# Kernel tuning notes

Hardware: AMD Instinct MI355X
Metric: run time of the kernel (lower is better)

The kernel has to match this reference:

```python
import jax, jax.numpy as jnp
import numpy as np

NUM_LAYERS = 4
INFERENCE_STEPS = 8
LR_STATE = 0.1
B, S, D, V = 8, 512, 1024, 32000


def setup_inputs() -> dict:
    key = jax.random.key(0)
    ks = jax.random.split(key, 8)
    input_ids = jax.random.randint(ks[0], (B, S), 0, V)
    targets = jax.random.randint(ks[1], (B, S), 0, V)
    emb = jax.random.normal(ks[2], (V, D), dtype=jnp.float32) * 0.02
    # torch init: randn(output_dim, input_dim) * sqrt(2/output_dim)
    W_stack = jax.random.normal(ks[3], (NUM_LAYERS, D, D), dtype=jnp.float32) * np.float32(np.sqrt(2.0 / D))
    b_stack = jnp.zeros((NUM_LAYERS, D), dtype=jnp.float32)
    out_W = jax.random.normal(ks[4], (V, D), dtype=jnp.float32) * 0.02
    out_b = jnp.zeros((V,), dtype=jnp.float32)
    # initialize_states: randn latent state per PC layer
    states_init = jax.random.normal(ks[5], (NUM_LAYERS, B, S, D), dtype=jnp.float32)
    return {"input_ids": input_ids, "targets": targets, "emb": emb,
            "W_stack": W_stack, "b_stack": b_stack, "out_W": out_W,
            "out_b": out_b, "states_init": states_init}


def _predict(mu_higher, W, b):
    # F.linear(mu_higher, W, b) = mu_higher @ W^T + b, W: [out_dim(in layer terms input_dim), in_dim]
    return jnp.einsum('bsj,ij->bsi', mu_higher, W) + b


def reference(input_ids, targets, emb, W_stack, b_stack, out_W, out_b, states_init):
    L = NUM_LAYERS
    x = emb[input_ids]  # [B,S,D] input embeds = states[0] (fixed)

    def step(states, _):
        mu = [x] + [states[i] for i in range(L)]
        grads = []
        for l in range(1, L + 1):
            Wl, bl = W_stack[l - 1], b_stack[l - 1]
            eps_lower = mu[l - 1] - _predict(mu[l], Wl, bl)
            # grad_from_below = -F.linear(eps, W.t()) = -eps @ W
            g = -jnp.einsum('bsi,ij->bsj', eps_lower, Wl)
            if l < L:
                eps_self = mu[l] - _predict(mu[l + 1], W_stack[l], b_stack[l])
                g = g + eps_self
            grads.append(g)
        new_states = jnp.stack([states[i] - LR_STATE * grads[i] for i in range(L)])
        return new_states, None

    states, _ = jax.lax.scan(step, states_init, None, length=INFERENCE_STEPS)

    mu = [x] + [states[i] for i in range(L)]
    pc_losses = [jnp.mean((mu[l] - _predict(mu[l + 1], W_stack[l], b_stack[l])) ** 2) for l in range(L)]
    pc_loss = jnp.mean(jnp.stack(pc_losses))

    logits = jnp.einsum('bsd,vd->bsv', states[L - 1][:, :-1, :], out_W) + out_b  # [B,S-1,V]
    tgt = targets[:, 1:]
    logp = jax.nn.log_softmax(logits, axis=-1)
    ce = -jnp.mean(jnp.take_along_axis(logp, tgt[..., None], axis=-1))
    return jnp.stack([ce, pc_loss])
```

## Files before the change

### kernel.cpp

```cpp
#include <hip/hip_runtime.h>

typedef unsigned short u16;
typedef __attribute__((ext_vector_type(8))) __bf16 bf16x8;
typedef __attribute__((ext_vector_type(4))) float floatx4;

#define NUM_LAYERS 4
#define STEPS 8
#define LRS 0.1f
#define M_ROWS 4096
#define D_DIM 1024
#define V_DIM 32000
#define KDIM 1024
#define SM ((size_t)M_ROWS * D_DIM)
#define WM ((size_t)D_DIM * D_DIM)

__device__ __forceinline__ u16 f2b(float f) {
    union { float f; unsigned u; } c; c.f = f;
    unsigned u = c.u;
    u = (u + 0x7FFFu + ((u >> 16) & 1u)) >> 16;
    return (u16)u;
}
__device__ __forceinline__ float b2f(u16 b) {
    union { unsigned u; float f; } c; c.u = ((unsigned)b) << 16;
    return c.f;
}
__device__ __forceinline__ unsigned pk2(float a, float b) {
    return (unsigned)f2b(a) | ((unsigned)f2b(b) << 16);
}

__device__ __forceinline__ void ld16(const u16* g, u16* l) {
    __builtin_amdgcn_global_load_lds(
        (const __attribute__((address_space(1))) void*)g,
        (__attribute__((address_space(3))) void*)l, 16, 0, 0);
}

__device__ __forceinline__ void gemm_core(const u16* __restrict__ A,
                                          const u16* __restrict__ B,
                                          int m0, int n0,
                                          floatx4 (&acc)[4][4],
                                          u16* smem) {
    u16* a_lds = smem;
    u16* b_lds = smem + 8192;
    const int tid  = threadIdx.x;
    const int lane = tid & 63;
    const int wave = tid >> 6;
    const int wm = wave >> 1, wn = wave & 1;
    const int q = lane >> 4, lr = lane & 15;
    const int qs = q ^ ((lr >> 1) & 3);

    const int r0 = wave * 16 + (lane >> 2);
    const int cc = ((lane & 3) ^ ((lane >> 3) & 3)) * 8;
    const u16* ga = A + ((size_t)(m0 + r0) << 10) + cc;
    const u16* gb = B + ((size_t)(n0 + r0) << 10) + cc;
    u16* la = &a_lds[wave * 512];
    u16* lb = &b_lds[wave * 512];

    #pragma unroll
    for (int i = 0; i < 4; i++)
        #pragma unroll
        for (int j = 0; j < 4; j++)
            acc[i][j] = floatx4{0.f, 0.f, 0.f, 0.f};

    for (int kt = 0; kt < KDIM; kt += 64) {
        __syncthreads();
        ld16(ga + kt,                   la);
        ld16(ga + kt + 32,              la + 4096);
        ld16(ga + (64 << 10) + kt,      la + 2048);
        ld16(ga + (64 << 10) + kt + 32, la + 2048 + 4096);
        ld16(gb + kt,                   lb);
        ld16(gb + kt + 32,              lb + 4096);
        ld16(gb + (64 << 10) + kt,      lb + 2048);
        ld16(gb + (64 << 10) + kt + 32, lb + 2048 + 4096);
        __syncthreads();
        #pragma unroll
        for (int h = 0; h < 2; h++) {
            bf16x8 bfv[4];
            #pragma unroll
            for (int ni = 0; ni < 4; ni++)
                bfv[ni] = *(const bf16x8*)
                    &b_lds[h * 4096 + (wn * 64 + ni * 16 + lr) * 32 + qs * 8];
            #pragma unroll
            for (int mi = 0; mi < 4; mi++) {
                bf16x8 a = *(const bf16x8*)
                    &a_lds[h * 4096 + (wm * 64 + mi * 16 + lr) * 32 + qs * 8];
                #pragma unroll
                for (int ni = 0; ni < 4; ni++)
                    acc[mi][ni] = __builtin_amdgcn_mfma_f32_16x16x32_bf16(
                        a, bfv[ni], acc[mi][ni], 0, 0, 0);
            }
        }
    }
}


__global__ __launch_bounds__(256, 4) void eps_gemm_k(
        const u16* __restrict__ sbf, const u16* __restrict__ Wbf,
        const u16* __restrict__ xbf, const float* __restrict__ b_stack,
        u16* __restrict__ epsb, float* __restrict__ pc_accum) {
    __shared__ __align__(16) u16 smem[16384];
    const int z = blockIdx.z;
    const int m0 = blockIdx.y * 128, n0 = blockIdx.x * 128;
    floatx4 acc[4][4];
    gemm_core(sbf + (size_t)z * SM, Wbf + (size_t)z * WM, m0, n0, acc, smem);
    const u16* lower = (z == 0) ? xbf : (sbf + (size_t)(z - 1) * SM);
    const float* bias = b_stack + z * D_DIM;
    u16* eo = epsb + (size_t)z * SM;
    const int tid = threadIdx.x, lane = tid & 63, wave = tid >> 6;
    const int wm = wave >> 1, wn = wave & 1, q = lane >> 4, lr = lane & 15;
    float sq = 0.f;
    #pragma unroll
    for (int mi = 0; mi < 4; mi++) {
        __syncthreads();
        #pragma unroll
        for (int ni = 0; ni < 4; ni++) {
            const int col = wn * 64 + ni * 16 + lr;
            const float bc = bias[n0 + col];
            #pragma unroll
            for (int r = 0; r < 4; r++) {
                const int row = wm * 16 + q * 4 + r;
                const int scn = ((col >> 3) + ((row >> 2) & 3) * 4) & 15;
                smem[row * 128 + scn * 8 + (col & 7)] = f2b(acc[mi][ni][r] + bc);
            }
        }
        __syncthreads();
        #pragma unroll
        for (int h = 0; h < 2; h++) {
            const int c = tid + h * 256;
            const int lrow = c >> 4, ch = c & 15;
            const int scn = (ch + ((lrow >> 2) & 3) * 4) & 15;
            const int grow = m0 + (lrow >> 4) * 64 + mi * 16 + (lrow & 15);
            const size_t gidx = (size_t)grow * D_DIM + n0 + ch * 8;
            bf16x8 st = *(const bf16x8*)&smem[lrow * 128 + scn * 8];
            bf16x8 lo = *(const bf16x8*)(lower + gidx);
            float e[8];
            #pragma unroll
            for (int i = 0; i < 8; i++) e[i] = (float)lo[i] - (float)st[i];
            if (pc_accum) {
                #pragma unroll
                for (int i = 0; i < 8; i++) sq += e[i] * e[i];
            } else {
                uint4 ov;
                ov.x = pk2(e[0], e[1]); ov.y = pk2(e[2], e[3]);
                ov.z = pk2(e[4], e[5]); ov.w = pk2(e[6], e[7]);
                *(uint4*)(eo + gidx) = ov;
            }
        }
    }
    if (pc_accum) {
        #pragma unroll
        for (int off = 1; off < 64; off <<= 1) sq += __shfl_xor(sq, off, 64);
        __shared__ float ls[4];
        if (lane == 0) ls[wave] = sq;
        __syncthreads();
        if (tid == 0) atomicAdd(pc_accum, ls[0] + ls[1] + ls[2] + ls[3]);
    }
}

__global__ __launch_bounds__(256, 4) void upd_gemm_k(
        const u16* __restrict__ epsb, const u16* __restrict__ WTbf,
        u16* __restrict__ sbf) {
    __shared__ __align__(16) u16 smem[16384];
    const int z = blockIdx.z;
    const int m0 = blockIdx.y * 128, n0 = blockIdx.x * 128;
    floatx4 acc[4][4];
    gemm_core(epsb + (size_t)z * SM, WTbf + (size_t)z * WM, m0, n0, acc, smem);
    u16* Sb = sbf + (size_t)z * SM;
    const bool hn = (z < 3);
    const u16* en = epsb + (size_t)(hn ? (z + 1) : z) * SM;
    const int tid = threadIdx.x, lane = tid & 63, wave = tid >> 6;
    const int wm = wave >> 1, wn = wave & 1, q = lane >> 4, lr = lane & 15;
    #pragma unroll
    for (int mi = 0; mi < 4; mi++) {
        __syncthreads();
        #pragma unroll
        for (int ni = 0; ni < 4; ni++) {
            const int col = wn * 64 + ni * 16 + lr;
            #pragma unroll
            for (int r = 0; r < 4; r++) {
                const int row = wm * 16 + q * 4 + r;
                const int scn = ((col >> 3) + ((row >> 2) & 3) * 4) & 15;
                smem[row * 128 + scn * 8 + (col & 7)] = f2b(LRS * acc[mi][ni][r]);
            }
        }
        __syncthreads();
        #pragma unroll
        for (int h = 0; h < 2; h++) {
            const int c = tid + h * 256;
            const int lrow = c >> 4, ch = c & 15;
            const int scn = (ch + ((lrow >> 2) & 3) * 4) & 15;
            const int grow = m0 + (lrow >> 4) * 64 + mi * 16 + (lrow & 15);
            const size_t gidx = (size_t)grow * D_DIM + n0 + ch * 8;
            bf16x8 st = *(const bf16x8*)&smem[lrow * 128 + scn * 8];
            bf16x8 S8 = *(const bf16x8*)(Sb + gidx);
            float v[8];
            #pragma unroll
            for (int i = 0; i < 8; i++) v[i] = (float)S8[i] + (float)st[i];
            if (hn) {
                bf16x8 e8 = *(const bf16x8*)(en + gidx);
                #pragma unroll
                for (int i = 0; i < 8; i++) v[i] -= LRS * (float)e8[i];
            }
            uint4 ov;
            ov.x = pk2(v[0], v[1]); ov.y = pk2(v[2], v[3]);
            ov.z = pk2(v[4], v[5]); ov.w = pk2(v[6], v[7]);
            *(uint4*)(Sb + gidx) = ov;
        }
    }
}

__global__ __launch_bounds__(256, 4) void logits_k(
        const u16* __restrict__ s4bf, const u16* __restrict__ oWb,
        const float* __restrict__ out_b, const int* __restrict__ targets,
        float* __restrict__ part_m, float* __restrict__ part_s,
        float* __restrict__ tlog) {
    __shared__ __align__(16) u16 smem[16384];
    const int m0 = blockIdx.x * 128, n0 = blockIdx.y * 128;
    floatx4 acc[4][4];
    gemm_core(s4bf, oWb, m0, n0, acc, smem);
    __shared__ float redm[128][2];
    __shared__ float reds[128][2];
    const int tid = threadIdx.x, lane = tid & 63, wave = tid >> 6;
    const int wm = wave >> 1, wn = wave & 1, q = lane >> 4, lr = lane & 15;
    float ob[4];
    #pragma unroll
    for (int ni = 0; ni < 4; ni++) ob[ni] = out_b[n0 + wn * 64 + ni * 16 + lr];
    #pragma unroll
    for (int mi = 0; mi < 4; mi++) {
        #pragma unroll
        for (int r = 0; r < 4; r++) {
            const int grow = m0 + wm * 64 + mi * 16 + q * 4 + r;
            float l[4];
            #pragma unroll
            for (int ni = 0; ni < 4; ni++) l[ni] = acc[mi][ni][r] + ob[ni];
            if ((grow & 511) != 511) {
                const int t = targets[grow + 1];
                #pragma unroll
                for (int ni = 0; ni < 4; ni++) {
                    const int gcol = n0 + wn * 64 + ni * 16 + lr;
                    if (t == gcol) tlog[grow] = l[ni];
                }
            }
            float mx = fmaxf(fmaxf(l[0], l[1]), fmaxf(l[2], l[3]));
            #pragma unroll
            for (int off = 1; off < 16; off <<= 1)
                mx = fmaxf(mx, __shfl_xor(mx, off, 64));
            float sm = __expf(l[0] - mx) + __expf(l[1] - mx) +
                       __expf(l[2] - mx) + __expf(l[3] - mx);
            #pragma unroll
            for (int off = 1; off < 16; off <<= 1)
                sm += __shfl_xor(sm, off, 64);
            if (lr == 0) {
                const int rrow = wm * 64 + mi * 16 + q * 4 + r;
                redm[rrow][wn] = mx;
                reds[rrow][wn] = sm;
            }
        }
    }
    __syncthreads();
    if (tid < 128) {
        float ma = redm[tid][0], mb = redm[tid][1];
        float M = fmaxf(ma, mb);
        float S = reds[tid][0] * __expf(ma - M) + reds[tid][1] * __expf(mb - M);
        part_m[(size_t)blockIdx.y * M_ROWS + m0 + tid] = M;
        part_s[(size_t)blockIdx.y * M_ROWS + m0 + tid] = S;
    }
}

__global__ void gather_k(const int* __restrict__ ids,
                         const float* __restrict__ emb,
                         u16* __restrict__ xbf) {
    const int row = blockIdx.x;
    const int c = threadIdx.x * 4;
    float4 v = *(const float4*)(emb + (size_t)ids[row] * D_DIM + c);
    uint2 o; o.x = pk2(v.x, v.y); o.y = pk2(v.z, v.w);
    *(uint2*)(xbf + (size_t)row * D_DIM + c) = o;
}

__global__ void conv_w_k(const float* __restrict__ W,
                         u16* __restrict__ Wbf, u16* __restrict__ WTbf) {
    __shared__ float t[32][33];
    const int z = blockIdx.z;
    const int i = blockIdx.y * 32 + threadIdx.y;
    const int j = blockIdx.x * 32 + threadIdx.x;
    const float v = W[(size_t)z * WM + (size_t)i * D_DIM + j];
    Wbf[(size_t)z * WM + (size_t)i * D_DIM + j] = f2b(v);
    t[threadIdx.y][threadIdx.x] = v;
    __syncthreads();
    const int jo = blockIdx.x * 32 + threadIdx.y;
    const int io = blockIdx.y * 32 + threadIdx.x;
    WTbf[(size_t)z * WM + (size_t)jo * D_DIM + io] = f2b(t[threadIdx.x][threadIdx.y]);
}

__global__ void conv_outw_k(const float* __restrict__ oW, u16* __restrict__ oWb) {
    const size_t i = ((size_t)blockIdx.x * 256 + threadIdx.x) * 4;
    float4 v = *(const float4*)(oW + i);
    uint2 o; o.x = pk2(v.x, v.y); o.y = pk2(v.z, v.w);
    *(uint2*)(oWb + i) = o;
}

__global__ void init_states_k(const float* __restrict__ si,
                              u16* __restrict__ sbf) {
    const size_t i = ((size_t)blockIdx.x * 256 + threadIdx.x) * 4;
    float4 v = *(const float4*)(si + i);
    uint2 o; o.x = pk2(v.x, v.y); o.y = pk2(v.z, v.w);
    *(uint2*)(sbf + i) = o;
}

__global__ void ce_reduce_k(const float* __restrict__ part_m,
                            const float* __restrict__ part_s,
                            const float* __restrict__ tlog,
                            float* __restrict__ ce_sum) {
    const int row = blockIdx.x;
    if ((row & 511) == 511) return;
    const int tid = threadIdx.x;
    const int NT = V_DIM / 128;
    float m = -3.0e38f;
    for (int nt = tid; nt < NT; nt += 256)
        m = fmaxf(m, part_m[(size_t)nt * M_ROWS + row]);
    #pragma unroll
    for (int off = 1; off < 64; off <<= 1) m = fmaxf(m, __shfl_xor(m, off, 64));
    __shared__ float sm[4], ss[4];
    if ((tid & 63) == 0) sm[tid >> 6] = m;
    __syncthreads();
    m = fmaxf(fmaxf(sm[0], sm[1]), fmaxf(sm[2], sm[3]));
    float s = 0.f;
    for (int nt = tid; nt < NT; nt += 256)
        s += part_s[(size_t)nt * M_ROWS + row] *
             __expf(part_m[(size_t)nt * M_ROWS + row] - m);
    #pragma unroll
    for (int off = 1; off < 64; off <<= 1) s += __shfl_xor(s, off, 64);
    if ((tid & 63) == 0) ss[tid >> 6] = s;
    __syncthreads();
    if (tid == 0) {
        float loss = m + __logf(ss[0] + ss[1] + ss[2] + ss[3]) - tlog[row];
        atomicAdd(ce_sum, loss);
    }
}

__global__ void finalize_k(const float* __restrict__ scal, float* __restrict__ out) {
    out[0] = scal[0] / 4088.0f;
    out[1] = scal[1] / (float)(4 * SM);
}

extern "C" void kernel_launch(void* const* d_in, const int* in_sizes, int n_in,
                              void* d_out, int out_size, void* d_ws, size_t ws_size,
                              hipStream_t stream) {
    (void)in_sizes; (void)n_in; (void)out_size; (void)ws_size;
    const int*   ids = (const int*)d_in[0];
    const int*   tgt = (const int*)d_in[1];
    const float* emb = (const float*)d_in[2];
    const float* W   = (const float*)d_in[3];
    const float* bs  = (const float*)d_in[4];
    const float* oW  = (const float*)d_in[5];
    const float* ob  = (const float*)d_in[6];
    const float* si  = (const float*)d_in[7];

    char* ws = (char*)d_ws;
    u16*   sbf    = (u16*)  (ws + 0);
    u16*   epsb   = (u16*)  (ws + 33554432);
    u16*   xbf    = (u16*)  (ws + 67108864);
    u16*   Wbf    = (u16*)  (ws + 75497472);
    u16*   WTbf   = (u16*)  (ws + 83886080);
    u16*   oWb    = (u16*)  (ws + 92274688);
    float* part_m = (float*)(ws + 157810688);
    float* part_s = (float*)(ws + 161906688);
    float* tlog   = (float*)(ws + 166002688);
    float* scal   = (float*)(ws + 166019072);

    hipMemsetAsync(scal, 0, 256, stream);
    gather_k<<<M_ROWS, 256, 0, stream>>>(ids, emb, xbf);
    conv_w_k<<<dim3(32, 32, 4), dim3(32, 32), 0, stream>>>(W, Wbf, WTbf);
    conv_outw_k<<<(V_DIM * D_DIM) / 1024, 256, 0, stream>>>(oW, oWb);
    init_states_k<<<(4 * (int)SM) / 1024, 256, 0, stream>>>(si, sbf);

    for (int step = 0; step < STEPS; ++step) {
        eps_gemm_k<<<dim3(8, 32, 4), 256, 0, stream>>>(sbf, Wbf, xbf, bs, epsb,
                                                       nullptr);
        upd_gemm_k<<<dim3(8, 32, 4), 256, 0, stream>>>(epsb, WTbf, sbf);
    }
    eps_gemm_k<<<dim3(8, 32, 4), 256, 0, stream>>>(sbf, Wbf, xbf, bs, epsb,
                                                   scal + 1);
    logits_k<<<dim3(32, V_DIM / 128), 256, 0, stream>>>(sbf + 3 * SM, oWb, ob, tgt,
                                                        part_m, part_s, tlog);
    ce_reduce_k<<<M_ROWS, 256, 0, stream>>>(part_m, part_s, tlog, scal);
    finalize_k<<<1, 1, 0, stream>>>(scal, (float*)d_out);
}
```

Measured before the change: 1.573 ms.

## Switch GEMMs to 256x256 tiles with double-buffered LDS ping-pong pipeline

Replaces the 128x128 single-buffered GEMM core with a 256x256-tile, 512-thread core. It double-buffers LDS via direct global-to-LDS loads and interleaves A/B sub-tile staging with MFMA phases, using barriers, setprio and explicit waitcnts. The goal is more data reuse per loaded byte and load latency hidden behind compute. Epilogues now go through an fp32 LDS slab instead of bf16, which drops one rounding step. Logits partials are reduced over 256-wide column tiles. The risk is that eps/upd grids shrink to 256 blocks with low occupancy per CU, and LDS use per block grows to 128KB.

```diff
diff --git a/kernel.cpp b/kernel.cpp
--- a/kernel.cpp
+++ b/kernel.cpp
@@ -11,6 +11,8 @@
 #define D_DIM 1024
 #define V_DIM 32000
 #define KDIM 1024
+#define NK 16
+#define NTV (V_DIM / 256)
 #define SM ((size_t)M_ROWS * D_DIM)
 #define WM ((size_t)D_DIM * D_DIM)
 
@@ -34,210 +36,278 @@
         (__attribute__((address_space(3))) void*)l, 16, 0, 0);
 }
 
-__device__ __forceinline__ void gemm_core(const u16* __restrict__ A,
-                                          const u16* __restrict__ B,
-                                          int m0, int n0,
-                                          floatx4 (&acc)[4][4],
-                                          u16* smem) {
-    u16* a_lds = smem;
-    u16* b_lds = smem + 8192;
+__device__ __forceinline__ void gemm256(const u16* __restrict__ A,
+                                        const u16* __restrict__ B,
+                                        int m0, int n0,
+                                        floatx4 (&acc)[8][4],
+                                        u16* __restrict__ smem) {
     const int tid  = threadIdx.x;
-    const int lane = tid & 63;
-    const int wave = tid >> 6;
-    const int wm = wave >> 1, wn = wave & 1;
+    const int lane = tid & 63, wave = tid >> 6;
+    const int wm = wave >> 2, wn = wave & 3;
     const int q = lane >> 4, lr = lane & 15;
-    const int qs = q ^ ((lr >> 1) & 3);
-
-    const int r0 = wave * 16 + (lane >> 2);
-    const int cc = ((lane & 3) ^ ((lane >> 3) & 3)) * 8;
-    const u16* ga = A + ((size_t)(m0 + r0) << 10) + cc;
-    const u16* gb = B + ((size_t)(n0 + r0) << 10) + cc;
-    u16* la = &a_lds[wave * 512];
-    u16* lb = &b_lds[wave * 512];
-
-    #pragma unroll
-    for (int i = 0; i < 4; i++)
+
+    const int sr = tid >> 3;
+    const int sc = ((tid & 7) ^ (sr & 7)) * 8;
+    const u16* gA = A + (size_t)(m0 + sr) * KDIM + sc;
+    const u16* gB = B + (size_t)(n0 + sr) * KDIM + sc;
+    const int ldsw = wave * 512;
+
+    const int arow = wm * 128 + lr;
+    const int brow = wn * 64 + lr;
+    const int ck0 = ((q) ^ (lr & 7)) * 8;
+    const int ck1 = ((4 + q) ^ (lr & 7)) * 8;
+
+    #pragma unroll
+    for (int i = 0; i < 8; i++)
         #pragma unroll
         for (int j = 0; j < 4; j++)
             acc[i][j] = floatx4{0.f, 0.f, 0.f, 0.f};
 
-    for (int kt = 0; kt < KDIM; kt += 64) {
-        __syncthreads();
-        ld16(ga + kt,                   la);
-        ld16(ga + kt + 32,              la + 4096);
-        ld16(ga + (64 << 10) + kt,      la + 2048);
-        ld16(ga + (64 << 10) + kt + 32, la + 2048 + 4096);
-        ld16(gb + kt,                   lb);
-        ld16(gb + kt + 32,              lb + 4096);
-        ld16(gb + (64 << 10) + kt,      lb + 2048);
-        ld16(gb + (64 << 10) + kt + 32, lb + 2048 + 4096);
-        __syncthreads();
-        #pragma unroll
-        for (int h = 0; h < 2; h++) {
-            bf16x8 bfv[4];
-            #pragma unroll
-            for (int ni = 0; ni < 4; ni++)
-                bfv[ni] = *(const bf16x8*)
-                    &b_lds[h * 4096 + (wn * 64 + ni * 16 + lr) * 32 + qs * 8];
-            #pragma unroll
-            for (int mi = 0; mi < 4; mi++) {
-                bf16x8 a = *(const bf16x8*)
-                    &a_lds[h * 4096 + (wm * 64 + mi * 16 + lr) * 32 + qs * 8];
-                #pragma unroll
-                for (int ni = 0; ni < 4; ni++)
-                    acc[mi][ni] = __builtin_amdgcn_mfma_f32_16x16x32_bf16(
-                        a, bfv[ni], acc[mi][ni], 0, 0, 0);
-            }
-        }
-    }
-}
-
-
-__global__ __launch_bounds__(256, 4) void eps_gemm_k(
+#define STG(bufb, isB, ah, tt) do {                                          \
+        const u16* g_ = ((isB) ? gB : gA)                                    \
+            + (size_t)((ah) * 128) * KDIM + (size_t)(tt) * 64;               \
+        u16* d_ = smem + (bufb) * 32768 + (isB) * 16384 + (ah) * 8192 + ldsw;\
+        ld16(g_, d_);                                                        \
+        ld16(g_ + (size_t)64 * KDIM, d_ + 4096);                             \
+    } while (0)
+#define LDA_(mi, ck) (*(const bf16x8*)&smem[bufo + (arow + (mi) * 16) * 64 + (ck)])
+#define LDB_(ni, ck) (*(const bf16x8*)&smem[bufo + 16384 + (brow + (ni) * 16) * 64 + (ck)])
+
+    STG(0, 0, 0, 0); STG(0, 0, 1, 0);
+    STG(0, 1, 0, 0); STG(0, 1, 1, 0);
+    STG(1, 1, 0, 1); STG(1, 1, 1, 1);
+    asm volatile("s_waitcnt vmcnt(4)" ::: "memory");
+    __builtin_amdgcn_s_barrier();
+    __builtin_amdgcn_sched_barrier(0);
+
+    bf16x8 af[4][2], bf[4][2];
+
+    #pragma unroll 2
+    for (int t = 0; t < NK; ++t) {
+        const int bufo = (t & 1) * 32768;
+        const int nb = (t + 1) & 1;
+        #pragma unroll
+        for (int i = 0; i < 4; i++) { af[i][0] = LDA_(i, ck0); af[i][1] = LDA_(i, ck1); }
+        #pragma unroll
+        for (int j = 0; j < 2; j++) { bf[j][0] = LDB_(j, ck0); bf[j][1] = LDB_(j, ck1); }
+        if (t + 1 < NK) STG(nb, 0, 0, t + 1);
+        __builtin_amdgcn_s_barrier();
+        asm volatile("s_waitcnt lgkmcnt(0)" ::: "memory");
+        __builtin_amdgcn_sched_barrier(0);
+        __builtin_amdgcn_s_setprio(1);
+        #pragma unroll
+        for (int i = 0; i < 4; i++)
+            #pragma unroll
+            for (int j = 0; j < 2; j++) {
+                acc[i][j] = __builtin_amdgcn_mfma_f32_16x16x32_bf16(af[i][0], bf[j][0], acc[i][j], 0, 0, 0);
+                acc[i][j] = __builtin_amdgcn_mfma_f32_16x16x32_bf16(af[i][1], bf[j][1], acc[i][j], 0, 0, 0);
+            }
+        __builtin_amdgcn_s_setprio(0);
+        __builtin_amdgcn_sched_barrier(0);
+        __builtin_amdgcn_s_barrier();
+        __builtin_amdgcn_sched_barrier(0);
+        #pragma unroll
+        for (int j = 2; j < 4; j++) { bf[j][0] = LDB_(j, ck0); bf[j][1] = LDB_(j, ck1); }
+        if (t + 1 < NK) STG(nb, 0, 1, t + 1);
+        __builtin_amdgcn_s_barrier();
+        asm volatile("s_waitcnt lgkmcnt(0)" ::: "memory");
+        __builtin_amdgcn_sched_barrier(0);
+        __builtin_amdgcn_s_setprio(1);
+        #pragma unroll
+        for (int i = 0; i < 4; i++)
+            #pragma unroll
+            for (int j = 2; j < 4; j++) {
+                acc[i][j] = __builtin_amdgcn_mfma_f32_16x16x32_bf16(af[i][0], bf[j][0], acc[i][j], 0, 0, 0);
+                acc[i][j] = __builtin_amdgcn_mfma_f32_16x16x32_bf16(af[i][1], bf[j][1], acc[i][j], 0, 0, 0);
+            }
+        __builtin_amdgcn_s_setprio(0);
+        __builtin_amdgcn_sched_barrier(0);
+        __builtin_amdgcn_s_barrier();
+        __builtin_amdgcn_sched_barrier(0);
+        #pragma unroll
+        for (int i = 0; i < 4; i++) { af[i][0] = LDA_(4 + i, ck0); af[i][1] = LDA_(4 + i, ck1); }
+        if (t + 2 < NK) STG(t & 1, 1, 0, t + 2);
+        __builtin_amdgcn_s_barrier();
+        asm volatile("s_waitcnt lgkmcnt(0)" ::: "memory");
+        __builtin_amdgcn_sched_barrier(0);
+        __builtin_amdgcn_s_setprio(1);
+        #pragma unroll
+        for (int i = 0; i < 4; i++)
+            #pragma unroll
+            for (int j = 0; j < 2; j++) {
+                acc[4 + i][j] = __builtin_amdgcn_mfma_f32_16x16x32_bf16(af[i][0], bf[j][0], acc[4 + i][j], 0, 0, 0);
+                acc[4 + i][j] = __builtin_amdgcn_mfma_f32_16x16x32_bf16(af[i][1], bf[j][1], acc[4 + i][j], 0, 0, 0);
+            }
+        __builtin_amdgcn_s_setprio(0);
+        __builtin_amdgcn_sched_barrier(0);
+        __builtin_amdgcn_s_barrier();
+        __builtin_amdgcn_sched_barrier(0);
+        if (t + 2 < NK) STG(t & 1, 1, 1, t + 2);
+        __builtin_amdgcn_s_barrier();
+        __builtin_amdgcn_sched_barrier(0);
+        __builtin_amdgcn_s_setprio(1);
+        #pragma unroll
+        for (int i = 0; i < 4; i++)
+            #pragma unroll
+            for (int j = 2; j < 4; j++) {
+                acc[4 + i][j] = __builtin_amdgcn_mfma_f32_16x16x32_bf16(af[i][0], bf[j][0], acc[4 + i][j], 0, 0, 0);
+                acc[4 + i][j] = __builtin_amdgcn_mfma_f32_16x16x32_bf16(af[i][1], bf[j][1], acc[4 + i][j], 0, 0, 0);
+            }
+        __builtin_amdgcn_s_setprio(0);
+        __builtin_amdgcn_sched_barrier(0);
+        if (t + 2 < NK) { asm volatile("s_waitcnt vmcnt(4)" ::: "memory"); }
+        else            { asm volatile("s_waitcnt vmcnt(0)" ::: "memory"); }
+        __builtin_amdgcn_s_barrier();
+        __builtin_amdgcn_sched_barrier(0);
+    }
+#undef STG
+#undef LDA_
+#undef LDB_
+}
+
+#define SLAB_S 68
+
+__global__ __launch_bounds__(512, 2) void eps_gemm_k(
         const u16* __restrict__ sbf, const u16* __restrict__ Wbf,
         const u16* __restrict__ xbf, const float* __restrict__ b_stack,
         u16* __restrict__ epsb, float* __restrict__ pc_accum) {
-    __shared__ __align__(16) u16 smem[16384];
+    __shared__ __align__(16) u16 smem[65536];
     const int z = blockIdx.z;
-    const int m0 = blockIdx.y * 128, n0 = blockIdx.x * 128;
-    floatx4 acc[4][4];
-    gemm_core(sbf + (size_t)z * SM, Wbf + (size_t)z * WM, m0, n0, acc, smem);
+    const int m0 = blockIdx.y * 256, n0 = blockIdx.x * 256;
+    floatx4 acc[8][4];
+    gemm256(sbf + (size_t)z * SM, Wbf + (size_t)z * WM, m0, n0, acc, smem);
     const u16* lower = (z == 0) ? xbf : (sbf + (size_t)(z - 1) * SM);
     const float* bias = b_stack + z * D_DIM;
     u16* eo = epsb + (size_t)z * SM;
     const int tid = threadIdx.x, lane = tid & 63, wave = tid >> 6;
-    const int wm = wave >> 1, wn = wave & 1, q = lane >> 4, lr = lane & 15;
+    const int wm = wave >> 2, wn = wave & 3, q = lane >> 4, lr = lane & 15;
+    float* fp = (float*)smem;
+    const int row2 = tid >> 1, scb = (tid & 1) * 32;
     float sq = 0.f;
     #pragma unroll
-    for (int mi = 0; mi < 4; mi++) {
-        __syncthreads();
-        #pragma unroll
-        for (int ni = 0; ni < 4; ni++) {
-            const int col = wn * 64 + ni * 16 + lr;
-            const float bc = bias[n0 + col];
-            #pragma unroll
-            for (int r = 0; r < 4; r++) {
-                const int row = wm * 16 + q * 4 + r;
-                const int scn = ((col >> 3) + ((row >> 2) & 3) * 4) & 15;
-                smem[row * 128 + scn * 8 + (col & 7)] = f2b(acc[mi][ni][r] + bc);
+    for (int ni = 0; ni < 4; ++ni) {
+        __syncthreads();
+        #pragma unroll
+        for (int mi = 0; mi < 8; ++mi)
+            #pragma unroll
+            for (int r = 0; r < 4; ++r)
+                fp[(wm * 128 + mi * 16 + q * 4 + r) * SLAB_S + wn * 16 + lr] = acc[mi][ni][r];
+        __syncthreads();
+        const int grow = m0 + row2;
+        #pragma unroll
+        for (int j = 0; j < 8; ++j) {
+            const int sc_ = scb + j * 4;
+            float4 v = *(const float4*)&fp[row2 * SLAB_S + sc_];
+            const int gcol = n0 + (sc_ >> 4) * 64 + ni * 16 + (sc_ & 15);
+            const size_t gidx = (size_t)grow * D_DIM + gcol;
+            const float4 b4 = *(const float4*)&bias[gcol];
+            ushort4 lo4 = *(const ushort4*)(lower + gidx);
+            float e0 = b2f(lo4.x) - (v.x + b4.x);
+            float e1 = b2f(lo4.y) - (v.y + b4.y);
+            float e2 = b2f(lo4.z) - (v.z + b4.z);
+            float e3 = b2f(lo4.w) - (v.w + b4.w);
+            if (pc_accum) {
+                sq += e0 * e0 + e1 * e1 + e2 * e2 + e3 * e3;
+            } else {
+                uint2 ov; ov.x = pk2(e0, e1); ov.y = pk2(e2, e3);
+                *(uint2*)(eo + gidx) = ov;
             }
         }
-        __syncthreads();
-        #pragma unroll
-        for (int h = 0; h < 2; h++) {
-            const int c = tid + h * 256;
-            const int lrow = c >> 4, ch = c & 15;
-            const int scn = (ch + ((lrow >> 2) & 3) * 4) & 15;
-            const int grow = m0 + (lrow >> 4) * 64 + mi * 16 + (lrow & 15);
-            const size_t gidx = (size_t)grow * D_DIM + n0 + ch * 8;
-            bf16x8 st = *(const bf16x8*)&smem[lrow * 128 + scn * 8];
-            bf16x8 lo = *(const bf16x8*)(lower + gidx);
-            float e[8];
-            #pragma unroll
-            for (int i = 0; i < 8; i++) e[i] = (float)lo[i] - (float)st[i];
-            if (pc_accum) {
-                #pragma unroll
-                for (int i = 0; i < 8; i++) sq += e[i] * e[i];
-            } else {
-                uint4 ov;
-                ov.x = pk2(e[0], e[1]); ov.y = pk2(e[2], e[3]);
-                ov.z = pk2(e[4], e[5]); ov.w = pk2(e[6], e[7]);
-                *(uint4*)(eo + gidx) = ov;
-            }
+    }
+    if (pc_accum) {
+        #pragma unroll
+        for (int off = 1; off < 64; off <<= 1) sq += __shfl_xor(sq, off, 64);
+        __syncthreads();
+        if (lane == 0) fp[wave] = sq;
+        __syncthreads();
+        if (tid == 0) {
+            float s = 0.f;
+            #pragma unroll
+            for (int w = 0; w < 8; ++w) s += fp[w];
+            atomicAdd(pc_accum, s);
         }
     }
-    if (pc_accum) {
-        #pragma unroll
-        for (int off = 1; off < 64; off <<= 1) sq += __shfl_xor(sq, off, 64);
-        __shared__ float ls[4];
-        if (lane == 0) ls[wave] = sq;
-        __syncthreads();
-        if (tid == 0) atomicAdd(pc_accum, ls[0] + ls[1] + ls[2] + ls[3]);
-    }
-}
-
-__global__ __launch_bounds__(256, 4) void upd_gemm_k(
+}
+
+__global__ __launch_bounds__(512, 2) void upd_gemm_k(
         const u16* __restrict__ epsb, const u16* __restrict__ WTbf,
         u16* __restrict__ sbf) {
-    __shared__ __align__(16) u16 smem[16384];
+    __shared__ __align__(16) u16 smem[65536];
     const int z = blockIdx.z;
-    const int m0 = blockIdx.y * 128, n0 = blockIdx.x * 128;
-    floatx4 acc[4][4];
-    gemm_core(epsb + (size_t)z * SM, WTbf + (size_t)z * WM, m0, n0, acc, smem);
+    const int m0 = blockIdx.y * 256, n0 = blockIdx.x * 256;
+    floatx4 acc[8][4];
+    gemm256(epsb + (size_t)z * SM, WTbf + (size_t)z * WM, m0, n0, acc, smem);
     u16* Sb = sbf + (size_t)z * SM;
     const bool hn = (z < 3);
     const u16* en = epsb + (size_t)(hn ? (z + 1) : z) * SM;
     const int tid = threadIdx.x, lane = tid & 63, wave = tid >> 6;
-    const int wm = wave >> 1, wn = wave & 1, q = lane >> 4, lr = lane & 15;
-    #pragma unroll
-    for (int mi = 0; mi < 4; mi++) {
-        __syncthreads();
-        #pragma unroll
-        for (int ni = 0; ni < 4; ni++) {
-            const int col = wn * 64 + ni * 16 + lr;
-            #pragma unroll
-            for (int r = 0; r < 4; r++) {
-                const int row = wm * 16 + q * 4 + r;
-                const int scn = ((col >> 3) + ((row >> 2) & 3) * 4) & 15;
-                smem[row * 128 + scn * 8 + (col & 7)] = f2b(LRS * acc[mi][ni][r]);
-            }
+    const int wm = wave >> 2, wn = wave & 3, q = lane >> 4, lr = lane & 15;
+    float* fp = (float*)smem;
+    const int row2 = tid >> 1, scb = (tid & 1) * 32;
+    #pragma unroll
+    for (int ni = 0; ni < 4; ++ni) {
+        __syncthreads();
+        #pragma unroll
+        for (int mi = 0; mi < 8; ++mi)
+            #pragma unroll
+            for (int r = 0; r < 4; ++r)
+                fp[(wm * 128 + mi * 16 + q * 4 + r) * SLAB_S + wn * 16 + lr] = acc[mi][ni][r];
+        __syncthreads();
+        const int grow = m0 + row2;
+        #pragma unroll
+        for (int j = 0; j < 8; ++j) {
+            const int sc_ = scb + j * 4;
+            float4 v = *(const float4*)&fp[row2 * SLAB_S + sc_];
+            const int gcol = n0 + (sc_ >> 4) * 64 + ni * 16 + (sc_ & 15);
+            const size_t gidx = (size_t)grow * D_DIM + gcol;
+            ushort4 S8 = *(const ushort4*)(Sb + gidx);
+            float v0 = b2f(S8.x) + LRS * v.x;
+            float v1 = b2f(S8.y) + LRS * v.y;
+            float v2 = b2f(S8.z) + LRS * v.z;
+            float v3 = b2f(S8.w) + LRS * v.w;
+            if (hn) {
+                ushort4 e8 = *(const ushort4*)(en + gidx);
+                v0 -= LRS * b2f(e8.x); v1 -= LRS * b2f(e8.y);
+                v2 -= LRS * b2f(e8.z); v3 -= LRS * b2f(e8.w);
+            }
+            uint2 ov; ov.x = pk2(v0, v1); ov.y = pk2(v2, v3);
+            *(uint2*)(Sb + gidx) = ov;
         }
-        __syncthreads();
-        #pragma unroll
-        for (int h = 0; h < 2; h++) {
-            const int c = tid + h * 256;
-            const int lrow = c >> 4, ch = c & 15;
-            const int scn = (ch + ((lrow >> 2) & 3) * 4) & 15;
-            const int grow = m0 + (lrow >> 4) * 64 + mi * 16 + (lrow & 15);
-            const size_t gidx = (size_t)grow * D_DIM + n0 + ch * 8;
-            bf16x8 st = *(const bf16x8*)&smem[lrow * 128 + scn * 8];
-            bf16x8 S8 = *(const bf16x8*)(Sb + gidx);
-            float v[8];
-            #pragma unroll
-            for (int i = 0; i < 8; i++) v[i] = (float)S8[i] + (float)st[i];
-            if (hn) {
-                bf16x8 e8 = *(const bf16x8*)(en + gidx);
-                #pragma unroll
-                for (int i = 0; i < 8; i++) v[i] -= LRS * (float)e8[i];
-            }
-            uint4 ov;
-            ov.x = pk2(v[0], v[1]); ov.y = pk2(v[2], v[3]);
-            ov.z = pk2(v[4], v[5]); ov.w = pk2(v[6], v[7]);
-            *(uint4*)(Sb + gidx) = ov;
-        }
-    }
-}
-
-__global__ __launch_bounds__(256, 4) void logits_k(
+    }
+}
+
+__global__ __launch_bounds__(512, 2) void logits_k(
         const u16* __restrict__ s4bf, const u16* __restrict__ oWb,
         const float* __restrict__ out_b, const int* __restrict__ targets,
         float* __restrict__ part_m, float* __restrict__ part_s,
         float* __restrict__ tlog) {
-    __shared__ __align__(16) u16 smem[16384];
-    const int m0 = blockIdx.x * 128, n0 = blockIdx.y * 128;
-    floatx4 acc[4][4];
-    gemm_core(s4bf, oWb, m0, n0, acc, smem);
-    __shared__ float redm[128][2];
-    __shared__ float reds[128][2];
+    __shared__ __align__(16) u16 smem[65536];
+    const int m0 = blockIdx.x * 256, n0 = blockIdx.y * 256;
+    floatx4 acc[8][4];
+    gemm256(s4bf, oWb, m0, n0, acc, smem);
     const int tid = threadIdx.x, lane = tid & 63, wave = tid >> 6;
-    const int wm = wave >> 1, wn = wave & 1, q = lane >> 4, lr = lane & 15;
+    const int wm = wave >> 2, wn = wave & 3, q = lane >> 4, lr = lane & 15;
+    float* redm = (float*)smem;
+    float* reds = redm + 1024;
     float ob[4];
     #pragma unroll
-    for (int ni = 0; ni < 4; ni++) ob[ni] = out_b[n0 + wn * 64 + ni * 16 + lr];
-    #pragma unroll
-    for (int mi = 0; mi < 4; mi++) {
-        #pragma unroll
-        for (int r = 0; r < 4; r++) {
-            const int grow = m0 + wm * 64 + mi * 16 + q * 4 + r;
+    for (int ni = 0; ni < 4; ++ni) ob[ni] = out_b[n0 + wn * 64 + ni * 16 + lr];
+    __syncthreads();
+    #pragma unroll
+    for (int mi = 0; mi < 8; ++mi) {
+        #pragma unroll
+        for (int r = 0; r < 4; ++r) {
+            const int rrow = wm * 128 + mi * 16 + q * 4 + r;
+            const int grow = m0 + rrow;
             float l[4];
             #pragma unroll
             for (int ni = 0; ni < 4; ni++) l[ni] = acc[mi][ni][r] + ob[ni];
             if ((grow & 511) != 511) {
-                const int t = targets[grow + 1];
+                const int tg = targets[grow + 1];
                 #pragma unroll
                 for (int ni = 0; ni < 4; ni++) {
                     const int gcol = n0 + wn * 64 + ni * 16 + lr;
-                    if (t == gcol) tlog[grow] = l[ni];
+                    if (tg == gcol) tlog[grow] = l[ni];
                 }
             }
             float mx = fmaxf(fmaxf(l[0], l[1]), fmaxf(l[2], l[3]));
@@ -249,18 +319,16 @@
             #pragma unroll
             for (int off = 1; off < 16; off <<= 1)
                 sm += __shfl_xor(sm, off, 64);
-            if (lr == 0) {
-                const int rrow = wm * 64 + mi * 16 + q * 4 + r;
-                redm[rrow][wn] = mx;
-                reds[rrow][wn] = sm;
-            }
+            if (lr == 0) { redm[rrow * 4 + wn] = mx; reds[rrow * 4 + wn] = sm; }
         }
     }
     __syncthreads();
-    if (tid < 128) {
-        float ma = redm[tid][0], mb = redm[tid][1];
-        float M = fmaxf(ma, mb);
-        float S = reds[tid][0] * __expf(ma - M) + reds[tid][1] * __expf(mb - M);
+    if (tid < 256) {
+        float ma = redm[tid * 4], mb = redm[tid * 4 + 1];
+        float mc = redm[tid * 4 + 2], md = redm[tid * 4 + 3];
+        float M = fmaxf(fmaxf(ma, mb), fmaxf(mc, md));
+        float S = reds[tid * 4] * __expf(ma - M) + reds[tid * 4 + 1] * __expf(mb - M)
+                + reds[tid * 4 + 2] * __expf(mc - M) + reds[tid * 4 + 3] * __expf(md - M);
         part_m[(size_t)blockIdx.y * M_ROWS + m0 + tid] = M;
         part_s[(size_t)blockIdx.y * M_ROWS + m0 + tid] = S;
     }
@@ -313,7 +381,7 @@
     const int row = blockIdx.x;
     if ((row & 511) == 511) return;
     const int tid = threadIdx.x;
-    const int NT = V_DIM / 128;
+    const int NT = NTV;
     float m = -3.0e38f;
     for (int nt = tid; nt < NT; nt += 256)
         m = fmaxf(m, part_m[(size_t)nt * M_ROWS + row]);
@@ -374,14 +442,14 @@
     init_states_k<<<(4 * (int)SM) / 1024, 256, 0, stream>>>(si, sbf);
 
     for (int step = 0; step < STEPS; ++step) {
-        eps_gemm_k<<<dim3(8, 32, 4), 256, 0, stream>>>(sbf, Wbf, xbf, bs, epsb,
+        eps_gemm_k<<<dim3(4, 16, 4), 512, 0, stream>>>(sbf, Wbf, xbf, bs, epsb,
                                                        nullptr);
-        upd_gemm_k<<<dim3(8, 32, 4), 256, 0, stream>>>(epsb, WTbf, sbf);
-    }
-    eps_gemm_k<<<dim3(8, 32, 4), 256, 0, stream>>>(sbf, Wbf, xbf, bs, epsb,
+        upd_gemm_k<<<dim3(4, 16, 4), 512, 0, stream>>>(epsb, WTbf, sbf);
+    }
+    eps_gemm_k<<<dim3(4, 16, 4), 512, 0, stream>>>(sbf, Wbf, xbf, bs, epsb,
                                                    scal + 1);
-    logits_k<<<dim3(32, V_DIM / 128), 256, 0, stream>>>(sbf + 3 * SM, oWb, ob, tgt,
-                                                        part_m, part_s, tlog);
+    logits_k<<<dim3(16, NTV), 512, 0, stream>>>(sbf + 3 * SM, oWb, ob, tgt,
+                                                part_m, part_s, tlog);
     ce_reduce_k<<<M_ROWS, 256, 0, stream>>>(part_m, part_s, tlog, scal);
     finalize_k<<<1, 1, 0, stream>>>(scal, (float*)d_out);
 }
```

Measured after the change: 3.058 ms. 1.94x slower.

## Use 256x256 pipelined GEMM tile with 512 threads for logits kernel

Applied to the files above, without the earlier changes.

Replaces the 128x128 logits GEMM with a new 256x256 tile core run by 8 waves. It double-buffers LDS at K-step 64, interleaves the global-to-LDS staging with MFMA phases, and raises wave priority during the MFMA phases. The larger tile increases operand reuse for the 4096x32000x1024 vocabulary projection, and the partial softmax reduction is adapted to 4 column waves. It uses 128KB of LDS per block and fewer, larger blocks, which lowers occupancy and risks a tail effect over the 16x125 grid.

```diff
diff --git a/kernel.cpp b/kernel.cpp
--- a/kernel.cpp
+++ b/kernel.cpp
@@ -11,6 +11,8 @@
 #define D_DIM 1024
 #define V_DIM 32000
 #define KDIM 1024
+#define NK 16
+#define NTV (V_DIM / 256)
 #define SM ((size_t)M_ROWS * D_DIM)
 #define WM ((size_t)D_DIM * D_DIM)
 
@@ -90,6 +92,119 @@
             }
         }
     }
+}
+
+__device__ __forceinline__ void gemm256(const u16* __restrict__ A,
+                                        const u16* __restrict__ B,
+                                        int m0, int n0,
+                                        floatx4 (&acc)[8][4],
+                                        u16* __restrict__ smem) {
+    const int tid  = threadIdx.x;
+    const int lane = tid & 63, wave = tid >> 6;
+    const int wm = wave >> 2, wn = wave & 3;
+    const int q = lane >> 4, lr = lane & 15;
+
+    const int sr = tid >> 3;
+    const int sc = ((tid & 7) ^ (sr & 7)) * 8;
+    const u16* gA = A + (size_t)(m0 + sr) * KDIM + sc;
+    const u16* gB = B + (size_t)(n0 + sr) * KDIM + sc;
+    const int ldsw = wave * 512;
+
+    const int arow = wm * 128 + lr;
+    const int brow = wn * 64 + lr;
+    const int ck0 = ((q) ^ (lr & 7)) * 8;
+    const int ck1 = ((4 + q) ^ (lr & 7)) * 8;
+
+    #pragma unroll
+    for (int i = 0; i < 8; i++)
+        #pragma unroll
+        for (int j = 0; j < 4; j++)
+            acc[i][j] = floatx4{0.f, 0.f, 0.f, 0.f};
+
+#define STG(bufb, isB, ah, tt) do {                                          \
+        const u16* g_ = ((isB) ? gB : gA)                                    \
+            + (size_t)((ah) * 128) * KDIM + (size_t)(tt) * 64;               \
+        u16* d_ = smem + (bufb) * 32768 + (isB) * 16384 + (ah) * 8192 + ldsw;\
+        ld16(g_, d_);                                                        \
+        ld16(g_ + (size_t)64 * KDIM, d_ + 4096);                             \
+    } while (0)
+#define LDA_(mi, ck) (*(const bf16x8*)&smem[bufo + (arow + (mi) * 16) * 64 + (ck)])
+#define LDB_(ni, ck) (*(const bf16x8*)&smem[bufo + 16384 + (brow + (ni) * 16) * 64 + (ck)])
+
+    STG(0, 0, 0, 0); STG(0, 0, 1, 0);
+    STG(0, 1, 0, 0); STG(0, 1, 1, 0);
+    STG(1, 1, 0, 1); STG(1, 1, 1, 1);
+    asm volatile("s_waitcnt vmcnt(4)" ::: "memory");
+    __builtin_amdgcn_s_barrier();
+
+    bf16x8 af[4][2], bf[4][2];
+
+    #pragma unroll 2
+    for (int t = 0; t < NK; ++t) {
+        const int bufo = (t & 1) * 32768;
+        const int nb = (t + 1) & 1;
+        #pragma unroll
+        for (int i = 0; i < 4; i++) { af[i][0] = LDA_(i, ck0); af[i][1] = LDA_(i, ck1); }
+        #pragma unroll
+        for (int j = 0; j < 2; j++) { bf[j][0] = LDB_(j, ck0); bf[j][1] = LDB_(j, ck1); }
+        if (t + 1 < NK) STG(nb, 0, 0, t + 1);
+        __builtin_amdgcn_s_barrier();
+        __builtin_amdgcn_s_setprio(1);
+        #pragma unroll
+        for (int i = 0; i < 4; i++)
+            #pragma unroll
+            for (int j = 0; j < 2; j++) {
+                acc[i][j] = __builtin_amdgcn_mfma_f32_16x16x32_bf16(af[i][0], bf[j][0], acc[i][j], 0, 0, 0);
+                acc[i][j] = __builtin_amdgcn_mfma_f32_16x16x32_bf16(af[i][1], bf[j][1], acc[i][j], 0, 0, 0);
+            }
+        __builtin_amdgcn_s_setprio(0);
+        __builtin_amdgcn_s_barrier();
+        #pragma unroll
+        for (int j = 2; j < 4; j++) { bf[j][0] = LDB_(j, ck0); bf[j][1] = LDB_(j, ck1); }
+        if (t + 1 < NK) STG(nb, 0, 1, t + 1);
+        __builtin_amdgcn_s_barrier();
+        __builtin_amdgcn_s_setprio(1);
+        #pragma unroll
+        for (int i = 0; i < 4; i++)
+            #pragma unroll
+            for (int j = 2; j < 4; j++) {
+                acc[i][j] = __builtin_amdgcn_mfma_f32_16x16x32_bf16(af[i][0], bf[j][0], acc[i][j], 0, 0, 0);
+                acc[i][j] = __builtin_amdgcn_mfma_f32_16x16x32_bf16(af[i][1], bf[j][1], acc[i][j], 0, 0, 0);
+            }
+        __builtin_amdgcn_s_setprio(0);
+        __builtin_amdgcn_s_barrier();
+        #pragma unroll
+        for (int i = 0; i < 4; i++) { af[i][0] = LDA_(4 + i, ck0); af[i][1] = LDA_(4 + i, ck1); }
+        if (t + 2 < NK) STG(t & 1, 1, 0, t + 2);
+        __builtin_amdgcn_s_barrier();
+        __builtin_amdgcn_s_setprio(1);
+        #pragma unroll
+        for (int i = 0; i < 4; i++)
+            #pragma unroll
+            for (int j = 0; j < 2; j++) {
+                acc[4 + i][j] = __builtin_amdgcn_mfma_f32_16x16x32_bf16(af[i][0], bf[j][0], acc[4 + i][j], 0, 0, 0);
+                acc[4 + i][j] = __builtin_amdgcn_mfma_f32_16x16x32_bf16(af[i][1], bf[j][1], acc[4 + i][j], 0, 0, 0);
+            }
+        __builtin_amdgcn_s_setprio(0);
+        __builtin_amdgcn_s_barrier();
+        if (t + 2 < NK) STG(t & 1, 1, 1, t + 2);
+        __builtin_amdgcn_s_barrier();
+        __builtin_amdgcn_s_setprio(1);
+        #pragma unroll
+        for (int i = 0; i < 4; i++)
+            #pragma unroll
+            for (int j = 2; j < 4; j++) {
+                acc[4 + i][j] = __builtin_amdgcn_mfma_f32_16x16x32_bf16(af[i][0], bf[j][0], acc[4 + i][j], 0, 0, 0);
+                acc[4 + i][j] = __builtin_amdgcn_mfma_f32_16x16x32_bf16(af[i][1], bf[j][1], acc[4 + i][j], 0, 0, 0);
+            }
+        __builtin_amdgcn_s_setprio(0);
+        if (t + 2 < NK) { asm volatile("s_waitcnt vmcnt(4)" ::: "memory"); }
+        else            { asm volatile("s_waitcnt vmcnt(0)" ::: "memory"); }
+        __builtin_amdgcn_s_barrier();
+    }
+#undef STG
+#undef LDA_
+#undef LDB_
 }
 
 
@@ -208,36 +323,38 @@
     }
 }
 
-__global__ __launch_bounds__(256, 4) void logits_k(
+__global__ __launch_bounds__(512, 2) void logits_k(
         const u16* __restrict__ s4bf, const u16* __restrict__ oWb,
         const float* __restrict__ out_b, const int* __restrict__ targets,
         float* __restrict__ part_m, float* __restrict__ part_s,
         float* __restrict__ tlog) {
-    __shared__ __align__(16) u16 smem[16384];
-    const int m0 = blockIdx.x * 128, n0 = blockIdx.y * 128;
-    floatx4 acc[4][4];
-    gemm_core(s4bf, oWb, m0, n0, acc, smem);
-    __shared__ float redm[128][2];
-    __shared__ float reds[128][2];
+    __shared__ __align__(16) u16 smem[65536];
+    const int m0 = blockIdx.x * 256, n0 = blockIdx.y * 256;
+    floatx4 acc[8][4];
+    gemm256(s4bf, oWb, m0, n0, acc, smem);
     const int tid = threadIdx.x, lane = tid & 63, wave = tid >> 6;
-    const int wm = wave >> 1, wn = wave & 1, q = lane >> 4, lr = lane & 15;
+    const int wm = wave >> 2, wn = wave & 3, q = lane >> 4, lr = lane & 15;
+    float* redm = (float*)smem;
+    float* reds = redm + 1024;
     float ob[4];
     #pragma unroll
-    for (int ni = 0; ni < 4; ni++) ob[ni] = out_b[n0 + wn * 64 + ni * 16 + lr];
-    #pragma unroll
-    for (int mi = 0; mi < 4; mi++) {
-        #pragma unroll
-        for (int r = 0; r < 4; r++) {
-            const int grow = m0 + wm * 64 + mi * 16 + q * 4 + r;
+    for (int ni = 0; ni < 4; ++ni) ob[ni] = out_b[n0 + wn * 64 + ni * 16 + lr];
+    __syncthreads();
+    #pragma unroll
+    for (int mi = 0; mi < 8; ++mi) {
+        #pragma unroll
+        for (int r = 0; r < 4; ++r) {
+            const int rrow = wm * 128 + mi * 16 + q * 4 + r;
+            const int grow = m0 + rrow;
             float l[4];
             #pragma unroll
             for (int ni = 0; ni < 4; ni++) l[ni] = acc[mi][ni][r] + ob[ni];
             if ((grow & 511) != 511) {
-                const int t = targets[grow + 1];
+                const int tg = targets[grow + 1];
                 #pragma unroll
                 for (int ni = 0; ni < 4; ni++) {
                     const int gcol = n0 + wn * 64 + ni * 16 + lr;
-                    if (t == gcol) tlog[grow] = l[ni];
+                    if (tg == gcol) tlog[grow] = l[ni];
                 }
             }
             float mx = fmaxf(fmaxf(l[0], l[1]), fmaxf(l[2], l[3]));
@@ -249,18 +366,16 @@
             #pragma unroll
             for (int off = 1; off < 16; off <<= 1)
                 sm += __shfl_xor(sm, off, 64);
-            if (lr == 0) {
-                const int rrow = wm * 64 + mi * 16 + q * 4 + r;
-                redm[rrow][wn] = mx;
-                reds[rrow][wn] = sm;
-            }
+            if (lr == 0) { redm[rrow * 4 + wn] = mx; reds[rrow * 4 + wn] = sm; }
         }
     }
     __syncthreads();
-    if (tid < 128) {
-        float ma = redm[tid][0], mb = redm[tid][1];
-        float M = fmaxf(ma, mb);
-        float S = reds[tid][0] * __expf(ma - M) + reds[tid][1] * __expf(mb - M);
+    if (tid < 256) {
+        float ma = redm[tid * 4], mb = redm[tid * 4 + 1];
+        float mc = redm[tid * 4 + 2], md = redm[tid * 4 + 3];
+        float M = fmaxf(fmaxf(ma, mb), fmaxf(mc, md));
+        float S = reds[tid * 4] * __expf(ma - M) + reds[tid * 4 + 1] * __expf(mb - M)
+                + reds[tid * 4 + 2] * __expf(mc - M) + reds[tid * 4 + 3] * __expf(md - M);
         part_m[(size_t)blockIdx.y * M_ROWS + m0 + tid] = M;
         part_s[(size_t)blockIdx.y * M_ROWS + m0 + tid] = S;
     }
@@ -313,7 +428,7 @@
     const int row = blockIdx.x;
     if ((row & 511) == 511) return;
     const int tid = threadIdx.x;
-    const int NT = V_DIM / 128;
+    const int NT = NTV;
     float m = -3.0e38f;
     for (int nt = tid; nt < NT; nt += 256)
         m = fmaxf(m, part_m[(size_t)nt * M_ROWS + row]);
@@ -380,8 +495,8 @@
     }
     eps_gemm_k<<<dim3(8, 32, 4), 256, 0, stream>>>(sbf, Wbf, xbf, bs, epsb,
                                                    scal + 1);
-    logits_k<<<dim3(32, V_DIM / 128), 256, 0, stream>>>(sbf + 3 * SM, oWb, ob, tgt,
-                                                        part_m, part_s, tlog);
+    logits_k<<<dim3(16, NTV), 512, 0, stream>>>(sbf + 3 * SM, oWb, ob, tgt,
+                                                part_m, part_s, tlog);
     ce_reduce_k<<<M_ROWS, 256, 0, stream>>>(part_m, part_s, tlog, scal);
     finalize_k<<<1, 1, 0, stream>>>(scal, (float*)d_out);
 }
```

New measurement: 1.585 ms. About the same (+0.8%).
